# Kernel tuning notes

Hardware: AMD Instinct MI355X
Metric: run time of the kernel (lower is better)

## Reference

```python
import jax, jax.numpy as jnp
import numpy as np

EPS = 1e-5

def _bn(x, g, b):
    # BatchNorm1d in training mode: biased batch variance, eps=1e-5
    mu = jnp.mean(x, axis=0)
    var = jnp.var(x, axis=0)
    return g * (x - mu) * jax.lax.rsqrt(var + EPS) + b

def _prelu(x, a):
    return jnp.where(x >= 0, x, a * x)

def setup_inputs() -> dict:
    key = jax.random.key(0)
    ks = jax.random.split(key, 32)
    B, MF, E = 4096, 128, 64
    f32 = jnp.float32

    def lin_w(k, o, i):
        bound = 1.0 / np.sqrt(i)
        return jax.random.uniform(k, (o, i), f32, -bound, bound)

    def lin_b(k, o, i):
        bound = 1.0 / np.sqrt(i)
        return jax.random.uniform(k, (o,), f32, -bound, bound)

    def exp_w(k, e, o, i):
        bound = 1.0 / np.sqrt(i)
        return jax.random.uniform(k, (e, o, i), f32, -bound, bound)

    def exp_b(k, e, o, i):
        bound = 1.0 / np.sqrt(i)
        return jax.random.uniform(k, (e, o), f32, -bound, bound)

    quarter = jnp.full((1,), 0.25, f32)  # PReLU default init
    return {
        'm0': jax.random.normal(ks[0], (B, MF), f32),
        'x0': jax.random.normal(ks[1], (B, 64), f32),
        'mW1': lin_w(ks[2], 256, 128), 'mb1': lin_b(ks[3], 256, 128),
        'mg1': jnp.ones((256,), f32), 'mbe1': jnp.zeros((256,), f32), 'ma1': quarter,
        'mW2': lin_w(ks[4], 128, 256), 'mb2': lin_b(ks[5], 128, 256),
        'mg2': jnp.ones((128,), f32), 'mbe2': jnp.zeros((128,), f32), 'ma2': quarter,
        'mW3': lin_w(ks[6], 64, 128), 'mb3': lin_b(ks[7], 64, 128),
        'mg3': jnp.ones((64,), f32), 'mbe3': jnp.zeros((64,), f32), 'ma3': quarter,
        'Wenc0': exp_w(ks[8], E, 256, 64), 'benc0': exp_b(ks[9], E, 256, 64),
        'Wenc1': exp_w(ks[10], E, 256, 256), 'benc1': exp_b(ks[11], E, 256, 256),
        'Wdec0': exp_w(ks[12], E, 256, 256), 'bdec0': exp_b(ks[13], E, 256, 256),
        'Wdec1': exp_w(ks[14], E, 64, 256), 'bdec1': exp_b(ks[15], E, 64, 256),
        'bng': jnp.ones((256,), f32), 'bnb': jnp.zeros((256,), f32), 'a': quarter,
    }

def reference(m0, x0, mW1, mb1, mg1, mbe1, ma1, mW2, mb2, mg2, mbe2, ma2,
              mW3, mb3, mg3, mbe3, ma3, Wenc0, benc0, Wenc1, benc1,
              Wdec0, bdec0, Wdec1, bdec1, bng, bnb, a):
    # m_encoder (MNet): Linear+BN+PReLU x3 -> per-sample expert weights [B, 64]
    h = _prelu(_bn(m0 @ mW1.T + mb1, mg1, mbe1), ma1)
    h = _prelu(_bn(h @ mW2.T + mb2, mg2, mbe2), ma2)
    w = _prelu(_bn(h @ mW3.T + mb3, mg3, mbe3), ma3)  # [B, E]

    w_sum = jnp.sum(w)           # scalar sum over all B*E, as in torch code
    wn = w / w_sum               # [B, E]

    def experts(z, W, b):
        # all-experts dense combine: sum_e wn[b,e] * (z @ W_e^T + b_e)
        h = jnp.einsum('bi,eoi->beo', z, W) + b  # [B, E, O]
        return jnp.einsum('beo,be->bo', h, wn)

    # encoder: depth=2, BN+PReLU after each layer (shared bn(256) and PReLU)
    z = _prelu(_bn(experts(x0, Wenc0, benc0), bng, bnb), a)
    z = _prelu(_bn(experts(z, Wenc1, benc1), bng, bnb), a)
    # decoder: BN+PReLU on all but last layer
    y = _prelu(_bn(experts(z, Wdec0, bdec0), bng, bnb), a)
    y = experts(y, Wdec1, bdec1)  # [B, 64]
    return y
```

## Files before the change

### kernel.cpp

```cpp
#include <hip/hip_runtime.h>
#include <stdint.h>

#define BATCH 4096
#define NEXP 64

typedef __bf16 bf16x8 __attribute__((ext_vector_type(8)));
typedef _Float16 f16x8 __attribute__((ext_vector_type(8)));
typedef float f32x4 __attribute__((ext_vector_type(4)));
typedef float f32x8 __attribute__((ext_vector_type(8)));
typedef unsigned int u32x4 __attribute__((ext_vector_type(4)));
typedef unsigned short u16x4 __attribute__((ext_vector_type(4)));
typedef unsigned short u16x8 __attribute__((ext_vector_type(8)));

__device__ __forceinline__ unsigned short f2bf(float f) {
  unsigned u = __builtin_bit_cast(unsigned, f);
  u += 0x7fffu + ((u >> 16) & 1u);
  return (unsigned short)(u >> 16);
}
__device__ __forceinline__ float bf2f(unsigned short h) {
  unsigned u = ((unsigned)h) << 16;
  return __builtin_bit_cast(float, u);
}
__device__ __forceinline__ unsigned short f2h(float f) {
  return __builtin_bit_cast(unsigned short, (_Float16)f);
}

__device__ __forceinline__ void async_copy16(const void* g, void* l) {
  __builtin_amdgcn_global_load_lds(
      (const __attribute__((address_space(1))) void*)(uintptr_t)g,
      (__attribute__((address_space(3))) void*)(uintptr_t)l, 16, 0, 0);
}

enum { AM_PLAIN = 0, AM_BN = 1 };

template <int BM_, int BN_, int WR, int WC, int AMODE>
__global__ __launch_bounds__(256, 4) void gemm_k(
    const float* __restrict__ Af32, const float* __restrict__ scv,
    const float* __restrict__ shv, const float* __restrict__ alphaPtr,
    const unsigned short* __restrict__ PB, int K, int nsubsTot,
    float* __restrict__ Cp, const float* __restrict__ biasv, int N,
    int ktilesTot) {
  constexpr int MS = BM_ / 16;
  constexpr int NS = BN_ / 16;
  constexpr int WTM = BM_ / WR, WTN = BN_ / WC;
  constexpr int TM = WTM / 16, TN = WTN / 16;
  constexpr int PCH = MS / 2;

  __shared__ __align__(16) unsigned short As[2 * MS * 512];
  __shared__ __align__(16) unsigned short Bs[2 * NS * 512];

  const int tid = threadIdx.x;
  const int lane = tid & 63;
  const int wid = tid >> 6;
  const int wrow = wid / WC, wcol = wid % WC;

  const int m0 = blockIdx.x * BM_;
  const int ntile = blockIdx.y;
  const int n0 = ntile * BN_;

  float alpha = 0.f;
  if constexpr (AMODE == AM_BN) alpha = alphaPtr[0];

  f32x4 acc[TM][TN] = {};

  for (int kt = 0; kt < ktilesTot; ++kt) {
    const int k0 = kt * 64;

    for (int f = wid; f < 2 * NS; f += 4) {
      const int fkt = f / NS, fns = f % NS;
      const long fragIdx = (long)(k0 / 32 + fkt) * nsubsTot + (ntile * NS + fns);
      async_copy16(PB + fragIdx * 512 + lane * 8, &Bs[f * 512 + lane * 8]);
    }

#pragma unroll
    for (int p = 0; p < PCH; ++p) {
      const int id = p * 256 + tid;
      const int fA = id >> 6;
      const int q = id & 63;
      const int ksh = fA / MS, msub = fA % MS;
      const int kq = q >> 4, mrow = q & 15;
      const int m = msub * 16 + mrow;
      const int kg = k0 + ksh * 32 + kq * 8;
      const long mg = m0 + m;
      f32x8 vf;
      if constexpr (AMODE == AM_PLAIN) {
        const f32x4* src = (const f32x4*)(Af32 + mg * K + kg);
        f32x4 a0 = src[0], a1 = src[1];
#pragma unroll
        for (int j = 0; j < 4; ++j) { vf[j] = a0[j]; vf[4 + j] = a1[j]; }
      } else {
        const f32x4* src = (const f32x4*)(Af32 + mg * K + kg);
        f32x4 a0 = src[0], a1 = src[1];
        f32x4 s0 = *(const f32x4*)(scv + kg), s1 = *(const f32x4*)(scv + kg + 4);
        f32x4 h0 = *(const f32x4*)(shv + kg), h1 = *(const f32x4*)(shv + kg + 4);
#pragma unroll
        for (int j = 0; j < 4; ++j) {
          float v = fmaf(a0[j], s0[j], h0[j]);
          vf[j] = v >= 0.f ? v : alpha * v;
          float v2 = fmaf(a1[j], s1[j], h1[j]);
          vf[4 + j] = v2 >= 0.f ? v2 : alpha * v2;
        }
      }
      bf16x8 ob = __builtin_convertvector(vf, bf16x8);
      *(u16x8*)&As[id * 8] = __builtin_bit_cast(u16x8, ob);
    }
    __syncthreads();

#pragma unroll
    for (int ks = 0; ks < 2; ++ks) {
      bf16x8 af[TM], bfr[TN];
#pragma unroll
      for (int i = 0; i < TM; ++i) {
        const int msub = wrow * TM + i;
        af[i] = __builtin_bit_cast(
            bf16x8, *(const u32x4*)&As[(ks * MS + msub) * 512 + lane * 8]);
      }
#pragma unroll
      for (int j = 0; j < TN; ++j) {
        const int nsub = wcol * TN + j;
        bfr[j] = __builtin_bit_cast(
            bf16x8, *(const u32x4*)&Bs[(ks * NS + nsub) * 512 + lane * 8]);
      }
#pragma unroll
      for (int i = 0; i < TM; ++i)
#pragma unroll
        for (int j = 0; j < TN; ++j)
          acc[i][j] = __builtin_amdgcn_mfma_f32_16x16x32_bf16(af[i], bfr[j],
                                                              acc[i][j], 0, 0, 0);
    }
    __syncthreads();
  }

  const int q = lane >> 4, nn = lane & 15;
#pragma unroll
  for (int i = 0; i < TM; ++i) {
    const int rowb = m0 + wrow * WTM + i * 16 + q * 4;
#pragma unroll
    for (int j = 0; j < TN; ++j) {
      const int col = n0 + wcol * WTN + j * 16 + nn;
      const float bv = biasv ? biasv[col] : 0.f;
#pragma unroll
      for (int r = 0; r < 4; ++r)
        Cp[(long)(rowb + r) * N + col] = acc[i][j][r] + bv;
    }
  }
}

template <int BN_, int KE_, int EPB, int NTILE, int KHALVES>
__global__ __launch_bounds__(256, 2) void egemm_k(
    const unsigned short* __restrict__ zpk, const float* __restrict__ wnT,
    const float* __restrict__ bias, const unsigned short* __restrict__ PB,
    float* __restrict__ Cbase, long partStride, int N, int nsubsTot) {
  constexpr int KT2F = KE_ / 32;
  constexpr int KT2 = KT2F / KHALVES;
  constexpr int LK = (KT2 == 8) ? 3 : (KT2 == 4) ? 2 : 1;
  constexpr int NS = BN_ / 16;
  constexpr int TN = NS / 4;
  constexpr int TM = 4;
  constexpr int S = NEXP / EPB;
  constexpr int NC = NTILE * S * KHALVES;
  constexpr int T = EPB * KT2;
  constexpr int U = ((KT2 & 3) == 0) ? 1 : (4 / KT2);

  __shared__ __align__(16) unsigned short As[KT2 * 4 * 512];

  const int tid = threadIdx.x, lane = tid & 63, wid = tid >> 6;
  const int bx = blockIdx.x;
  const int combo = bx % NC;
  const int mb = bx / NC;
  const int ntile = combo % NTILE;
  const int rest = combo / NTILE;
  const int slice = rest % S;
  const int khalf = rest / S;
  const int e0 = slice * EPB;
  const int n0 = ntile * BN_;
  float* __restrict__ Cp = Cbase + (long)(khalf * S + slice) * partStride;
  const int nn = lane & 15, q = lane >> 4;
  const bool addBias = (KHALVES == 1) || (khalf == 0);

  {
    const unsigned short* zb =
        zpk + (long)mb * (KT2F * 4 * 512) + (long)khalf * (KT2 * 4 * 512);
    for (int f = wid; f < KT2 * 4; f += 4)
      async_copy16(zb + f * 512 + lane * 8, &As[f * 512 + lane * 8]);
  }

  const long kstr = (long)nsubsTot * 512;
  const unsigned short* Bq = PB + ((long)e0 * KT2F + khalf * KT2) * kstr +
                             ((long)ntile * NS + wid * TN) * 512 + lane * 8;
  auto baddr = [&](int u) {
    const int ei = u >> LK, kt = u & (KT2 - 1);
    return Bq + ((long)ei * KT2F + kt) * kstr;
  };

  u32x4 ring[4][TN];
#pragma unroll
  for (int t = 0; t < 4; ++t) {
    const unsigned short* a = baddr(t < T ? t : T - 1);
#pragma unroll
    for (int j = 0; j < TN; ++j) ring[t][j] = *(const u32x4*)(a + j * 512);
  }

  __syncthreads();

  f32x4 mainAcc[TM][TN] = {};

  for (int eb = 0; eb < EPB; eb += U) {
#pragma unroll
    for (int uu = 0; uu < U; ++uu) {
      const int ei = eb + uu;
      const int e = e0 + ei;
      f32x4 tmp[TM][TN];
#pragma unroll
      for (int j = 0; j < TN; ++j) {
        const float bv =
            addBias ? bias[(long)e * N + n0 + wid * (TN * 16) + j * 16 + nn]
                    : 0.f;
        f32x4 t4 = {bv, bv, bv, bv};
#pragma unroll
        for (int i = 0; i < TM; ++i) tmp[i][j] = t4;
      }
#pragma unroll
      for (int kt = 0; kt < KT2; ++kt) {
        const int slot = (uu * KT2 + kt) & 3;
#pragma unroll
        for (int i = 0; i < TM; ++i) {
          f16x8 af = __builtin_bit_cast(
              f16x8, *(const u32x4*)&As[(kt * 4 + i) * 512 + lane * 8]);
#pragma unroll
          for (int j = 0; j < TN; ++j)
            tmp[i][j] = __builtin_amdgcn_mfma_f32_16x16x32_f16(
                af, __builtin_bit_cast(f16x8, ring[slot][j]), tmp[i][j], 0, 0,
                0);
        }
        {
          const int u = ei * KT2 + kt;
          const int un = (u + 4 < T) ? (u + 4) : (T - 1);
          const unsigned short* a = baddr(un);
#pragma unroll
          for (int j = 0; j < TN; ++j)
            ring[slot][j] = *(const u32x4*)(a + j * 512);
        }
      }
#pragma unroll
      for (int i = 0; i < TM; ++i) {
        const int rowb = mb * 64 + i * 16 + q * 4;
        f32x4 wn4 = *(const f32x4*)(wnT + (long)e * BATCH + rowb);
#pragma unroll
        for (int j = 0; j < TN; ++j) mainAcc[i][j] += wn4 * tmp[i][j];
      }
    }
  }

#pragma unroll
  for (int i = 0; i < TM; ++i) {
    const int rowb = mb * 64 + i * 16 + q * 4;
#pragma unroll
    for (int j = 0; j < TN; ++j) {
      const int col = n0 + wid * (TN * 16) + j * 16 + nn;
#pragma unroll
      for (int r = 0; r < 4; ++r)
        Cp[(long)(rowb + r) * N + col] = mainAcc[i][j][r];
    }
  }
}

template <int EPB>
__global__ __launch_bounds__(256, 1) void egemm2_k(
    const unsigned short* __restrict__ zpk, const float* __restrict__ wnT,
    const float* __restrict__ bias, const unsigned short* __restrict__ PB,
    unsigned short* __restrict__ Pb, long partStrideH) {
  constexpr int TM = 8, TN = 4;
  constexpr int S = NEXP / EPB;
  constexpr int T = EPB * 8;

  __shared__ __align__(16) unsigned short As[8 * 8 * 512];

  const int tid = threadIdx.x, lane = tid & 63, wid = tid >> 6;
  const int bx = blockIdx.x;
  const int slice = bx % S;
  const int mb = bx / S;
  const int e0 = slice * EPB;
  const int nn = lane & 15, q = lane >> 4;

  for (int f = wid; f < 64; f += 4) {
    const int kt = f >> 3, msub = f & 7;
    const unsigned short* src =
        zpk + ((long)(2 * mb + (msub >> 2)) * 32 + kt * 4 + (msub & 3)) * 512;
    async_copy16(src + lane * 8, &As[f * 512 + lane * 8]);
  }

  const long kstr = 16L * 512;
  const unsigned short* Bq =
      PB + (long)e0 * 8 * kstr + ((long)wid * TN) * 512 + lane * 8;

  u32x4 ring[4][TN];
#pragma unroll
  for (int t = 0; t < 4; ++t)
#pragma unroll
    for (int j = 0; j < TN; ++j)
      ring[t][j] = *(const u32x4*)(Bq + (long)t * kstr + j * 512);

  __syncthreads();

  f32x4 acc[TM][TN] = {};

  for (int ei = 0; ei < EPB; ++ei) {
    const int e = e0 + ei;
    f16x8 wnh[TM];
#pragma unroll
    for (int i = 0; i < TM; ++i) {
      const float w =
          wnT[(long)e * BATCH + mb * 128 + i * 16 + (lane & 15)] * 4096.f;
      const _Float16 h = (_Float16)w;
      f16x8 v = {h, h, h, h, h, h, h, h};
      wnh[i] = v;
    }
#pragma unroll
    for (int kt = 0; kt < 8; ++kt) {
      const int slot = kt & 3;
#pragma unroll
      for (int i = 0; i < TM; ++i) {
        f16x8 af = __builtin_bit_cast(
            f16x8, *(const u32x4*)&As[(kt * 8 + i) * 512 + lane * 8]);
        f16x8 afs = af * wnh[i];
#pragma unroll
        for (int j = 0; j < TN; ++j)
          acc[i][j] = __builtin_amdgcn_mfma_f32_16x16x32_f16(
              afs, __builtin_bit_cast(f16x8, ring[slot][j]), acc[i][j], 0, 0,
              0);
      }
      {
        const int u = ei * 8 + kt;
        const int un = (u + 4 < T) ? (u + 4) : (T - 1);
#pragma unroll
        for (int j = 0; j < TN; ++j)
          ring[slot][j] = *(const u32x4*)(Bq + (long)un * kstr + j * 512);
      }
    }
  }

#pragma unroll
  for (int i = 0; i < TM; ++i)
#pragma unroll
    for (int j = 0; j < TN; ++j) acc[i][j] *= (1.f / 4096.f);
  for (int ei = 0; ei < EPB; ++ei) {
    const int e = e0 + ei;
    float bs[TN];
#pragma unroll
    for (int j = 0; j < TN; ++j)
      bs[j] = bias[(long)e * 256 + wid * 64 + j * 16 + nn];
#pragma unroll
    for (int i = 0; i < TM; ++i) {
      f32x4 wn4 =
          *(const f32x4*)(wnT + (long)e * BATCH + mb * 128 + i * 16 + q * 4);
#pragma unroll
      for (int j = 0; j < TN; ++j) acc[i][j] += wn4 * bs[j];
    }
  }
  unsigned short* Cp = Pb + (long)slice * partStrideH;
#pragma unroll
  for (int i = 0; i < TM; ++i) {
    const int rowb = mb * 128 + i * 16 + q * 4;
#pragma unroll
    for (int j = 0; j < TN; ++j) {
      const int col = wid * 64 + j * 16 + nn;
#pragma unroll
      for (int r = 0; r < 4; ++r)
        Cp[(long)(rowb + r) * 256 + col] = f2bf(acc[i][j][r]);
    }
  }
}

template <int NPARTS>
__global__ void hstats_k(float* __restrict__ P, long partStride,
                         f32x4* __restrict__ BS1, f32x4* __restrict__ BS2) {
  const int c0 = (threadIdx.x & 63) * 4;
  const int rg = threadIdx.x >> 6;
  const int rb = blockIdx.x * 8;
  f32x4 s = {0.f, 0.f, 0.f, 0.f}, s2 = {0.f, 0.f, 0.f, 0.f};
#pragma unroll
  for (int it = 0; it < 2; ++it) {
    const long r = rb + it * 4 + rg;
    f32x4 v[NPARTS];
#pragma unroll
    for (int p = 0; p < NPARTS; ++p)
      v[p] = *(const f32x4*)(P + p * partStride + r * 256 + c0);
    f32x4 x = v[0];
#pragma unroll
    for (int p = 1; p < NPARTS; ++p) x += v[p];
    *(f32x4*)(P + r * 256 + c0) = x;
    s += x;
    s2 += x * x;
  }
  __shared__ f32x4 sb[256], qb[256];
  sb[threadIdx.x] = s;
  qb[threadIdx.x] = s2;
  __syncthreads();
  if (threadIdx.x < 64) {
    f32x4 ts = sb[threadIdx.x] + sb[64 + threadIdx.x] + sb[128 + threadIdx.x] +
               sb[192 + threadIdx.x];
    f32x4 tq = qb[threadIdx.x] + qb[64 + threadIdx.x] + qb[128 + threadIdx.x] +
               qb[192 + threadIdx.x];
    BS1[threadIdx.x * 512 + blockIdx.x] = ts;
    BS2[threadIdx.x * 512 + blockIdx.x] = tq;
  }
}

__global__ void hstats16_k(const unsigned short* __restrict__ P,
                           long partStrideH, float* __restrict__ H,
                           f32x4* __restrict__ BS1, f32x4* __restrict__ BS2) {
  const int c0 = (threadIdx.x & 63) * 4;
  const int rg = threadIdx.x >> 6;
  const int rb = blockIdx.x * 8;
  f32x4 s = {0.f, 0.f, 0.f, 0.f}, s2 = {0.f, 0.f, 0.f, 0.f};
#pragma unroll
  for (int it = 0; it < 2; ++it) {
    const long r = rb + it * 4 + rg;
    u16x4 v[8];
#pragma unroll
    for (int p = 0; p < 8; ++p)
      v[p] = *(const u16x4*)(P + p * partStrideH + r * 256 + c0);
    f32x4 x = {0.f, 0.f, 0.f, 0.f};
#pragma unroll
    for (int p = 0; p < 8; ++p)
#pragma unroll
      for (int j = 0; j < 4; ++j) x[j] += bf2f(v[p][j]);
    *(f32x4*)(H + r * 256 + c0) = x;
    s += x;
    s2 += x * x;
  }
  __shared__ f32x4 sb[256], qb[256];
  sb[threadIdx.x] = s;
  qb[threadIdx.x] = s2;
  __syncthreads();
  if (threadIdx.x < 64) {
    f32x4 ts = sb[threadIdx.x] + sb[64 + threadIdx.x] + sb[128 + threadIdx.x] +
               sb[192 + threadIdx.x];
    f32x4 tq = qb[threadIdx.x] + qb[64 + threadIdx.x] + qb[128 + threadIdx.x] +
               qb[192 + threadIdx.x];
    BS1[threadIdx.x * 512 + blockIdx.x] = ts;
    BS2[threadIdx.x * 512 + blockIdx.x] = tq;
  }
}

__global__ void sfin_k(const f32x4* __restrict__ BS1,
                       const f32x4* __restrict__ BS2,
                       const float* __restrict__ g, const float* __restrict__ b,
                       float* __restrict__ scv, float* __restrict__ shv) {
  const int cg = blockIdx.x;
  f32x4 s1 = BS1[cg * 512 + threadIdx.x] + BS1[cg * 512 + 256 + threadIdx.x];
  f32x4 s2 = BS2[cg * 512 + threadIdx.x] + BS2[cg * 512 + 256 + threadIdx.x];
  __shared__ f32x4 sb[256], qb[256];
  sb[threadIdx.x] = s1;
  qb[threadIdx.x] = s2;
  __syncthreads();
  for (int st = 128; st > 0; st >>= 1) {
    if (threadIdx.x < st) {
      sb[threadIdx.x] += sb[threadIdx.x + st];
      qb[threadIdx.x] += qb[threadIdx.x + st];
    }
    __syncthreads();
  }
  if (threadIdx.x < 4) {
    const int c = cg * 4 + threadIdx.x;
    float mu = sb[0][threadIdx.x] * (1.f / BATCH);
    float var = qb[0][threadIdx.x] * (1.f / BATCH) - mu * mu;
    float isig = 1.f / sqrtf(var + 1e-5f);
    float sc_ = g[c] * isig;
    scv[c] = sc_;
    shv[c] = b[c] - mu * sc_;
  }
}

__global__ void stats_k(const float* __restrict__ H, int C,
                        const float* __restrict__ g, const float* __restrict__ b,
                        float* __restrict__ scv, float* __restrict__ shv) {
  const int c0 = blockIdx.x * 4;
  f32x4 s = {0.f, 0.f, 0.f, 0.f}, s2 = {0.f, 0.f, 0.f, 0.f};
  for (int r = threadIdx.x; r < BATCH; r += 256) {
    f32x4 x = *(const f32x4*)(H + (long)r * C + c0);
    s += x;
    s2 += x * x;
  }
  __shared__ f32x4 sb[256], qb[256];
  sb[threadIdx.x] = s;
  qb[threadIdx.x] = s2;
  __syncthreads();
  for (int st = 128; st > 0; st >>= 1) {
    if (threadIdx.x < st) {
      sb[threadIdx.x] += sb[threadIdx.x + st];
      qb[threadIdx.x] += qb[threadIdx.x + st];
    }
    __syncthreads();
  }
  if (threadIdx.x < 4) {
    const int c = c0 + threadIdx.x;
    float mu = sb[0][threadIdx.x] * (1.f / BATCH);
    float var = qb[0][threadIdx.x] * (1.f / BATCH) - mu * mu;
    float isig = 1.f / sqrtf(var + 1e-5f);
    float sc_ = g[c] * isig;
    scv[c] = sc_;
    shv[c] = b[c] - mu * sc_;
  }
}

__global__ void zbuild_pk(const float* __restrict__ H,
                          const float* __restrict__ scv,
                          const float* __restrict__ shv,
                          const float* __restrict__ alphaPtr,
                          unsigned short* __restrict__ zpk) {
  const int c = blockIdx.x * 256 + threadIdx.x;
  const float alpha = alphaPtr[0];
  const int mb = c >> 11, r = c & 2047;
  const int kt = r >> 8, q2 = r & 255;
  const int msub = q2 >> 6, ln = q2 & 63;
  const int row = mb * 64 + msub * 16 + (ln & 15);
  const int col = kt * 32 + (ln >> 4) * 8;
  const float* src = H + (long)row * 256 + col;
  f32x4 a0 = *(const f32x4*)src, a1 = *(const f32x4*)(src + 4);
  f32x4 s0 = *(const f32x4*)(scv + col), s1 = *(const f32x4*)(scv + col + 4);
  f32x4 h0 = *(const f32x4*)(shv + col), h1 = *(const f32x4*)(shv + col + 4);
  u16x8 o;
#pragma unroll
  for (int j = 0; j < 4; ++j) {
    float v = fmaf(a0[j], s0[j], h0[j]);
    v = v >= 0.f ? v : alpha * v;
    o[j] = f2h(v);
    float v2 = fmaf(a1[j], s1[j], h1[j]);
    v2 = v2 >= 0.f ? v2 : alpha * v2;
    o[4 + j] = f2h(v2);
  }
  *(u16x8*)(zpk + (long)c * 8) = o;
}

__global__ void wbuild_k(const float* __restrict__ G, const float* __restrict__ scv,
                         const float* __restrict__ shv,
                         const float* __restrict__ alphaPtr,
                         float* __restrict__ w, float* __restrict__ wps) {
  const int idx = blockIdx.x * 256 + threadIdx.x;
  const float alpha = alphaPtr[0];
  const int c0 = (idx * 4) & 63;
  f32x4 x = *(const f32x4*)(G + (long)idx * 4);
  f32x4 sv = *(const f32x4*)(scv + c0);
  f32x4 hv = *(const f32x4*)(shv + c0);
  f32x4 o;
  float part = 0.f;
#pragma unroll
  for (int j = 0; j < 4; ++j) {
    float v = fmaf(x[j], sv[j], hv[j]);
    v = v >= 0.f ? v : alpha * v;
    o[j] = v;
    part += v;
  }
  *(f32x4*)(w + (long)idx * 4) = o;
  __shared__ float sb[256];
  sb[threadIdx.x] = part;
  __syncthreads();
  for (int st = 128; st > 0; st >>= 1) {
    if (threadIdx.x < st) sb[threadIdx.x] += sb[threadIdx.x + st];
    __syncthreads();
  }
  if (threadIdx.x == 0) wps[blockIdx.x] = sb[0];
}

__global__ void wnTcast_k(const float* __restrict__ w,
                          const float* __restrict__ wps,
                          float* __restrict__ wnT, const float* __restrict__ x0,
                          unsigned short* __restrict__ x0pk) {
  const int bx = blockIdx.x;
  if (bx < 1024) {
    __shared__ float sb[256];
    sb[threadIdx.x] = wps[threadIdx.x];
    __syncthreads();
    for (int st = 128; st > 0; st >>= 1) {
      if (threadIdx.x < st) sb[threadIdx.x] += sb[threadIdx.x + st];
      __syncthreads();
    }
    const float inv = 1.0f / sb[0];
    const int idx = bx * 256 + threadIdx.x;
    const int e = idx >> 12, b2 = idx & 4095;
    wnT[idx] = w[(long)b2 * NEXP + e] * inv;
  } else {
    const int c = (bx - 1024) * 256 + threadIdx.x;
    const int mb = c >> 9, r = c & 511;
    const int kt = r >> 8, q2 = r & 255;
    const int msub = q2 >> 6, ln = q2 & 63;
    const int row = mb * 64 + msub * 16 + (ln & 15);
    const int col = kt * 32 + (ln >> 4) * 8;
    const float* src = x0 + (long)row * 64 + col;
    f32x4 a0 = *(const f32x4*)src, a1 = *(const f32x4*)(src + 4);
    u16x8 o;
#pragma unroll
    for (int j = 0; j < 4; ++j) {
      o[j] = f2h(a0[j]);
      o[4 + j] = f2h(a1[j]);
    }
    *(u16x8*)(x0pk + (long)c * 8) = o;
  }
}

__global__ void mnetprep_k(const float* __restrict__ w0,
                           const float* __restrict__ w1,
                           const float* __restrict__ w2,
                           unsigned short* __restrict__ PB) {
  const int t = blockIdx.x * 256 + threadIdx.x;
  const float* W;
  int nsubs, shI;
  long loc;
  if (t < 4096) { W = w0; nsubs = 16; shI = 7; loc = t; }
  else if (t < 8192) { W = w1; nsubs = 8; shI = 8; loc = t - 4096; }
  else if (t < 9216) { W = w2; nsubs = 4; shI = 7; loc = t - 8192; }
  else return;
  const int lane = (int)(loc & 63);
  const long frag = loc >> 6;
  const int nsub = (int)(frag % nsubs);
  const long ktile = frag / nsubs;
  const int n = nsub * 16 + (lane & 15);
  const int k = (int)(ktile * 32 + (lane >> 4) * 8);
  const int e = k >> shI;
  const int i0 = k & ((1 << shI) - 1);
  const int O = nsubs * 16;
  const float* src = W + ((long)e * O + n) * (1 << shI) + i0;
  f32x4 a0 = *(const f32x4*)src, a1 = *(const f32x4*)(src + 4);
  u16x8 o;
#pragma unroll
  for (int j = 0; j < 4; ++j) {
    o[j] = f2bf(a0[j]);
    o[4 + j] = f2bf(a1[j]);
  }
  *(u16x8*)(PB + (long)t * 8) = o;
}

__global__ void eprep_k(const float* __restrict__ W,
                        unsigned short* __restrict__ PB, int nsubs, int shI,
                        long totalChunks) {
  const long t = (long)blockIdx.x * 256 + threadIdx.x;
  if (t >= totalChunks) return;
  const int lane = (int)(t & 63);
  const long frag = t >> 6;
  const int nsub = (int)(frag % nsubs);
  const long ktile = frag / nsubs;
  const int n = nsub * 16 + (lane & 15);
  const int k = (int)(ktile * 32 + (lane >> 4) * 8);
  const int e = k >> shI;
  const int i0 = k & ((1 << shI) - 1);
  const int O = nsubs * 16;
  const float* src = W + ((long)e * O + n) * (1 << shI) + i0;
  f32x4 a0 = *(const f32x4*)src, a1 = *(const f32x4*)(src + 4);
  u16x8 o;
#pragma unroll
  for (int j = 0; j < 4; ++j) {
    o[j] = f2h(a0[j]);
    o[4 + j] = f2h(a1[j]);
  }
  *(u16x8*)(PB + (long)t * 8) = o;
}

template <int NP>
__global__ void reduceN_k(const float* __restrict__ P, long partStride,
                          float* __restrict__ out, int total4) {
  const int idx = blockIdx.x * 256 + threadIdx.x;
  if (idx >= total4) return;
  f32x4 v[NP];
#pragma unroll
  for (int p = 0; p < NP; ++p)
    v[p] = *(const f32x4*)(P + p * partStride + (long)idx * 4);
  f32x4 s = v[0];
#pragma unroll
  for (int p = 1; p < NP; ++p) s += v[p];
  *(f32x4*)(out + (long)idx * 4) = s;
}

extern "C" void kernel_launch(void* const* d_in, const int* in_sizes, int n_in,
                              void* d_out, int out_size, void* d_ws, size_t ws_size,
                              hipStream_t stream) {
  const float* m0 = (const float*)d_in[0];
  const float* x0 = (const float*)d_in[1];
  const float* mW1 = (const float*)d_in[2];
  const float* mb1 = (const float*)d_in[3];
  const float* mg1 = (const float*)d_in[4];
  const float* mbe1 = (const float*)d_in[5];
  const float* ma1 = (const float*)d_in[6];
  const float* mW2 = (const float*)d_in[7];
  const float* mb2 = (const float*)d_in[8];
  const float* mg2 = (const float*)d_in[9];
  const float* mbe2 = (const float*)d_in[10];
  const float* ma2 = (const float*)d_in[11];
  const float* mW3 = (const float*)d_in[12];
  const float* mb3 = (const float*)d_in[13];
  const float* mg3 = (const float*)d_in[14];
  const float* mbe3 = (const float*)d_in[15];
  const float* ma3 = (const float*)d_in[16];
  const float* Wenc0 = (const float*)d_in[17];
  const float* benc0 = (const float*)d_in[18];
  const float* Wenc1 = (const float*)d_in[19];
  const float* benc1 = (const float*)d_in[20];
  const float* Wdec0 = (const float*)d_in[21];
  const float* bdec0 = (const float*)d_in[22];
  const float* Wdec1 = (const float*)d_in[23];
  const float* bdec1 = (const float*)d_in[24];
  const float* bng = (const float*)d_in[25];
  const float* bnb = (const float*)d_in[26];
  const float* aexp = (const float*)d_in[27];

  const long PSP32 = (long)BATCH * 256 + 64;
  const long PSPH = (long)BATCH * 256 + 128;
  const long PSD = (long)BATCH * 64 + 64;

  char* base = (char*)d_ws;
  size_t off = 0;
  auto alloc = [&](size_t bytes) {
    void* p = base + off;
    off = (off + bytes + 255) & ~(size_t)255;
    return p;
  };
  unsigned short* PBm = (unsigned short*)alloc(9216L * 16);
  unsigned short* PBe = (unsigned short*)alloc(524288L * 16);
  size_t pbBytes = 16UL * PSD * 4;
  if (8UL * PSPH * 2 > pbBytes) pbBytes = 8UL * PSPH * 2;
  if (4UL * PSP32 * 4 > pbBytes) pbBytes = 4UL * PSP32 * 4;
  void* PbBase = alloc(pbBytes);
  float* Pb32 = (float*)PbBase;
  unsigned short* Pb16 = (unsigned short*)PbBase;
  float* P0 = Pb32;
  float* P1 = Pb32 + (long)BATCH * 256;
  float* Hbuf = (float*)alloc((size_t)BATCH * 256 * 4);
  unsigned short* zApk = (unsigned short*)alloc(BATCH * 256 * 2);
  unsigned short* zBpk = (unsigned short*)alloc(BATCH * 256 * 2);
  unsigned short* x0pk = (unsigned short*)alloc(BATCH * 64 * 2);
  float* wbuf = (float*)alloc(BATCH * 64 * 4);
  float* wnT = (float*)alloc((size_t)NEXP * BATCH * 4);
  f32x4* BS1 = (f32x4*)alloc(64 * 512 * 16);
  f32x4* BS2 = (f32x4*)alloc(64 * 512 * 16);
  float* scv = (float*)alloc(256 * 4);
  float* shv = (float*)alloc(256 * 4);
  float* wps = (float*)alloc(256 * 4);

  const dim3 blk(256);

  mnetprep_k<<<36, blk, 0, stream>>>(mW1, mW2, mW3, PBm);

  gemm_k<64, 128, 2, 2, AM_PLAIN><<<dim3(64, 2, 1), blk, 0, stream>>>(
      m0, nullptr, nullptr, nullptr, PBm, 128, 16, P0, mb1, 256, 2);
  stats_k<<<64, blk, 0, stream>>>(P0, 256, mg1, mbe1, scv, shv);
  gemm_k<64, 128, 2, 2, AM_BN><<<dim3(64, 1, 1), blk, 0, stream>>>(
      P0, scv, shv, ma1, PBm + 4096L * 8, 256, 8, P1, mb2, 128, 4);
  stats_k<<<32, blk, 0, stream>>>(P1, 128, mg2, mbe2, scv, shv);
  gemm_k<64, 64, 2, 2, AM_BN><<<dim3(64, 1, 1), blk, 0, stream>>>(
      P1, scv, shv, ma2, PBm + 8192L * 8, 128, 4, P0, mb3, 64, 2);
  stats_k<<<16, blk, 0, stream>>>(P0, 64, mg3, mbe3, scv, shv);
  wbuild_k<<<256, blk, 0, stream>>>(P0, scv, shv, ma3, wbuf, wps);
  wnTcast_k<<<1152, blk, 0, stream>>>(wbuf, wps, wnT, x0, x0pk);

  eprep_k<<<512, blk, 0, stream>>>(Wenc0, PBe, 16, 6, 131072);
  egemm_k<128, 64, 16, 2, 1><<<dim3(512), blk, 0, stream>>>(
      x0pk, wnT, benc0, PBe, Pb32, PSP32, 256, 16);
  hstats_k<4><<<512, blk, 0, stream>>>(Pb32, PSP32, BS1, BS2);
  sfin_k<<<64, blk, 0, stream>>>(BS1, BS2, bng, bnb, scv, shv);
  zbuild_pk<<<512, blk, 0, stream>>>(Pb32, scv, shv, aexp, zApk);

  eprep_k<<<2048, blk, 0, stream>>>(Wenc1, PBe, 16, 8, 524288);
  egemm2_k<8><<<dim3(256), blk, 0, stream>>>(zApk, wnT, benc1, PBe, Pb16, PSPH);
  hstats16_k<<<512, blk, 0, stream>>>(Pb16, PSPH, Hbuf, BS1, BS2);
  sfin_k<<<64, blk, 0, stream>>>(BS1, BS2, bng, bnb, scv, shv);
  zbuild_pk<<<512, blk, 0, stream>>>(Hbuf, scv, shv, aexp, zBpk);

  eprep_k<<<2048, blk, 0, stream>>>(Wdec0, PBe, 16, 8, 524288);
  egemm2_k<8><<<dim3(256), blk, 0, stream>>>(zBpk, wnT, bdec0, PBe, Pb16, PSPH);
  hstats16_k<<<512, blk, 0, stream>>>(Pb16, PSPH, Hbuf, BS1, BS2);
  sfin_k<<<64, blk, 0, stream>>>(BS1, BS2, bng, bnb, scv, shv);
  zbuild_pk<<<512, blk, 0, stream>>>(Hbuf, scv, shv, aexp, zApk);

  eprep_k<<<512, blk, 0, stream>>>(Wdec1, PBe, 4, 8, 131072);
  egemm_k<64, 256, 8, 1, 2><<<dim3(1024), blk, 0, stream>>>(
      zApk, wnT, bdec1, PBe, Pb32, PSD, 64, 4);
  reduceN_k<16><<<256, blk, 0, stream>>>(Pb32, PSD, (float*)d_out, 65536);

  (void)in_sizes; (void)n_in; (void)out_size; (void)ws_size;
}
```

Baseline: 358.9 us.

## Split egemm2 K dimension across blocks and fuse partial reduction into zbuild

Result: slower. 471.2 us (+31.3%).

```diff
diff --git a/kernel.cpp b/kernel.cpp
--- a/kernel.cpp
+++ b/kernel.cpp
@@ -265,41 +265,49 @@
   }
 }
 
-template <int EPB>
-__global__ __launch_bounds__(256, 1) void egemm2_k(
+__global__ __launch_bounds__(256, 2) void egemm2_k(
     const unsigned short* __restrict__ zpk, const float* __restrict__ wnT,
     const float* __restrict__ bias, const unsigned short* __restrict__ PB,
     unsigned short* __restrict__ Pb, long partStrideH) {
   constexpr int TM = 8, TN = 4;
-  constexpr int S = NEXP / EPB;
-  constexpr int T = EPB * 8;
-
-  __shared__ __align__(16) unsigned short As[8 * 8 * 512];
+  constexpr int EPB = 8, S = 8;
+  constexpr int NC = S * 2;
+  constexpr int T = EPB * 4;
+
+  __shared__ __align__(16) unsigned short As[4 * 8 * 512];
 
   const int tid = threadIdx.x, lane = tid & 63, wid = tid >> 6;
   const int bx = blockIdx.x;
-  const int slice = bx % S;
-  const int mb = bx / S;
+  const int combo = bx % NC;
+  const int mb = bx / NC;
+  const int slice = combo % S;
+  const int khalf = combo / S;
   const int e0 = slice * EPB;
   const int nn = lane & 15, q = lane >> 4;
 
-  for (int f = wid; f < 64; f += 4) {
+  for (int f = wid; f < 32; f += 4) {
     const int kt = f >> 3, msub = f & 7;
+    const int ktg = khalf * 4 + kt;
     const unsigned short* src =
-        zpk + ((long)(2 * mb + (msub >> 2)) * 32 + kt * 4 + (msub & 3)) * 512;
+        zpk + ((long)(2 * mb + (msub >> 2)) * 32 + ktg * 4 + (msub & 3)) * 512;
     async_copy16(src + lane * 8, &As[f * 512 + lane * 8]);
   }
 
   const long kstr = 16L * 512;
-  const unsigned short* Bq =
-      PB + (long)e0 * 8 * kstr + ((long)wid * TN) * 512 + lane * 8;
+  const unsigned short* Bq = PB + ((long)e0 * 8 + khalf * 4) * kstr +
+                             ((long)wid * TN) * 512 + lane * 8;
+  auto baddr = [&](int u) {
+    const int ei = u >> 2, kt = u & 3;
+    return Bq + ((long)ei * 8 + kt) * kstr;
+  };
 
   u32x4 ring[4][TN];
 #pragma unroll
-  for (int t = 0; t < 4; ++t)
-#pragma unroll
-    for (int j = 0; j < TN; ++j)
-      ring[t][j] = *(const u32x4*)(Bq + (long)t * kstr + j * 512);
+  for (int t = 0; t < 4; ++t) {
+    const unsigned short* a = baddr(t);
+#pragma unroll
+    for (int j = 0; j < TN; ++j) ring[t][j] = *(const u32x4*)(a + j * 512);
+  }
 
   __syncthreads();
 
@@ -310,15 +318,14 @@
     f16x8 wnh[TM];
 #pragma unroll
     for (int i = 0; i < TM; ++i) {
-      const float w =
-          wnT[(long)e * BATCH + mb * 128 + i * 16 + (lane & 15)] * 4096.f;
+      const float w = wnT[(long)e * BATCH + mb * 128 + i * 16 + nn] * 4096.f;
       const _Float16 h = (_Float16)w;
       f16x8 v = {h, h, h, h, h, h, h, h};
       wnh[i] = v;
     }
 #pragma unroll
-    for (int kt = 0; kt < 8; ++kt) {
-      const int slot = kt & 3;
+    for (int kt = 0; kt < 4; ++kt) {
+      const int slot = kt;
 #pragma unroll
       for (int i = 0; i < TM; ++i) {
         f16x8 af = __builtin_bit_cast(
@@ -331,11 +338,12 @@
               0);
       }
       {
-        const int u = ei * 8 + kt;
+        const int u = ei * 4 + kt;
         const int un = (u + 4 < T) ? (u + 4) : (T - 1);
+        const unsigned short* a = baddr(un);
 #pragma unroll
         for (int j = 0; j < TN; ++j)
-          ring[slot][j] = *(const u32x4*)(Bq + (long)un * kstr + j * 512);
+          ring[slot][j] = *(const u32x4*)(a + j * 512);
       }
     }
   }
@@ -344,21 +352,23 @@
   for (int i = 0; i < TM; ++i)
 #pragma unroll
     for (int j = 0; j < TN; ++j) acc[i][j] *= (1.f / 4096.f);
-  for (int ei = 0; ei < EPB; ++ei) {
-    const int e = e0 + ei;
-    float bs[TN];
-#pragma unroll
-    for (int j = 0; j < TN; ++j)
-      bs[j] = bias[(long)e * 256 + wid * 64 + j * 16 + nn];
-#pragma unroll
-    for (int i = 0; i < TM; ++i) {
-      f32x4 wn4 =
-          *(const f32x4*)(wnT + (long)e * BATCH + mb * 128 + i * 16 + q * 4);
-#pragma unroll
-      for (int j = 0; j < TN; ++j) acc[i][j] += wn4 * bs[j];
-    }
-  }
-  unsigned short* Cp = Pb + (long)slice * partStrideH;
+  if (khalf == 0) {
+    for (int ei = 0; ei < EPB; ++ei) {
+      const int e = e0 + ei;
+      float bs[TN];
+#pragma unroll
+      for (int j = 0; j < TN; ++j)
+        bs[j] = bias[(long)e * 256 + wid * 64 + j * 16 + nn];
+#pragma unroll
+      for (int i = 0; i < TM; ++i) {
+        f32x4 wn4 =
+            *(const f32x4*)(wnT + (long)e * BATCH + mb * 128 + i * 16 + q * 4);
+#pragma unroll
+        for (int j = 0; j < TN; ++j) acc[i][j] += wn4 * bs[j];
+      }
+    }
+  }
+  unsigned short* Cp = Pb + (long)(khalf * S + slice) * partStrideH;
 #pragma unroll
   for (int i = 0; i < TM; ++i) {
     const int rowb = mb * 128 + i * 16 + q * 4;
@@ -408,8 +418,8 @@
 }
 
 __global__ void hstats16_k(const unsigned short* __restrict__ P,
-                           long partStrideH, float* __restrict__ H,
-                           f32x4* __restrict__ BS1, f32x4* __restrict__ BS2) {
+                           long partStrideH, f32x4* __restrict__ BS1,
+                           f32x4* __restrict__ BS2) {
   const int c0 = (threadIdx.x & 63) * 4;
   const int rg = threadIdx.x >> 6;
   const int rb = blockIdx.x * 8;
@@ -417,16 +427,15 @@
 #pragma unroll
   for (int it = 0; it < 2; ++it) {
     const long r = rb + it * 4 + rg;
-    u16x4 v[8];
-#pragma unroll
-    for (int p = 0; p < 8; ++p)
+    u16x4 v[16];
+#pragma unroll
+    for (int p = 0; p < 16; ++p)
       v[p] = *(const u16x4*)(P + p * partStrideH + r * 256 + c0);
     f32x4 x = {0.f, 0.f, 0.f, 0.f};
 #pragma unroll
-    for (int p = 0; p < 8; ++p)
+    for (int p = 0; p < 16; ++p)
 #pragma unroll
       for (int j = 0; j < 4; ++j) x[j] += bf2f(v[p][j]);
-    *(f32x4*)(H + r * 256 + c0) = x;
     s += x;
     s2 += x * x;
   }
@@ -528,6 +537,41 @@
     v = v >= 0.f ? v : alpha * v;
     o[j] = f2h(v);
     float v2 = fmaf(a1[j], s1[j], h1[j]);
+    v2 = v2 >= 0.f ? v2 : alpha * v2;
+    o[4 + j] = f2h(v2);
+  }
+  *(u16x8*)(zpk + (long)c * 8) = o;
+}
+
+__global__ void zbuild16_pk(const unsigned short* __restrict__ P,
+                            long partStrideH, const float* __restrict__ scv,
+                            const float* __restrict__ shv,
+                            const float* __restrict__ alphaPtr,
+                            unsigned short* __restrict__ zpk) {
+  const int c = blockIdx.x * 256 + threadIdx.x;
+  const float alpha = alphaPtr[0];
+  const int mb = c >> 11, r = c & 2047;
+  const int kt = r >> 8, q2 = r & 255;
+  const int msub = q2 >> 6, ln = q2 & 63;
+  const int row = mb * 64 + msub * 16 + (ln & 15);
+  const int col = kt * 32 + (ln >> 4) * 8;
+  const long base = (long)row * 256 + col;
+  float s[8] = {0.f, 0.f, 0.f, 0.f, 0.f, 0.f, 0.f, 0.f};
+#pragma unroll
+  for (int p = 0; p < 16; ++p) {
+    u16x8 v = *(const u16x8*)(P + p * partStrideH + base);
+#pragma unroll
+    for (int j = 0; j < 8; ++j) s[j] += bf2f(v[j]);
+  }
+  f32x4 s0 = *(const f32x4*)(scv + col), s1 = *(const f32x4*)(scv + col + 4);
+  f32x4 h0 = *(const f32x4*)(shv + col), h1 = *(const f32x4*)(shv + col + 4);
+  u16x8 o;
+#pragma unroll
+  for (int j = 0; j < 4; ++j) {
+    float v = fmaf(s[j], s0[j], h0[j]);
+    v = v >= 0.f ? v : alpha * v;
+    o[j] = f2h(v);
+    float v2 = fmaf(s[4 + j], s1[j], h1[j]);
     v2 = v2 >= 0.f ? v2 : alpha * v2;
     o[4 + j] = f2h(v2);
   }
@@ -717,15 +761,14 @@
   };
   unsigned short* PBm = (unsigned short*)alloc(9216L * 16);
   unsigned short* PBe = (unsigned short*)alloc(524288L * 16);
-  size_t pbBytes = 16UL * PSD * 4;
-  if (8UL * PSPH * 2 > pbBytes) pbBytes = 8UL * PSPH * 2;
+  size_t pbBytes = 16UL * PSPH * 2;
   if (4UL * PSP32 * 4 > pbBytes) pbBytes = 4UL * PSP32 * 4;
+  if (16UL * PSD * 4 > pbBytes) pbBytes = 16UL * PSD * 4;
   void* PbBase = alloc(pbBytes);
   float* Pb32 = (float*)PbBase;
   unsigned short* Pb16 = (unsigned short*)PbBase;
   float* P0 = Pb32;
   float* P1 = Pb32 + (long)BATCH * 256;
-  float* Hbuf = (float*)alloc((size_t)BATCH * 256 * 4);
   unsigned short* zApk = (unsigned short*)alloc(BATCH * 256 * 2);
   unsigned short* zBpk = (unsigned short*)alloc(BATCH * 256 * 2);
   unsigned short* x0pk = (unsigned short*)alloc(BATCH * 64 * 2);
@@ -761,16 +804,16 @@
   zbuild_pk<<<512, blk, 0, stream>>>(Pb32, scv, shv, aexp, zApk);
 
   eprep_k<<<2048, blk, 0, stream>>>(Wenc1, PBe, 16, 8, 524288);
-  egemm2_k<8><<<dim3(256), blk, 0, stream>>>(zApk, wnT, benc1, PBe, Pb16, PSPH);
-  hstats16_k<<<512, blk, 0, stream>>>(Pb16, PSPH, Hbuf, BS1, BS2);
+  egemm2_k<<<dim3(512), blk, 0, stream>>>(zApk, wnT, benc1, PBe, Pb16, PSPH);
+  hstats16_k<<<512, blk, 0, stream>>>(Pb16, PSPH, BS1, BS2);
   sfin_k<<<64, blk, 0, stream>>>(BS1, BS2, bng, bnb, scv, shv);
-  zbuild_pk<<<512, blk, 0, stream>>>(Hbuf, scv, shv, aexp, zBpk);
+  zbuild16_pk<<<512, blk, 0, stream>>>(Pb16, PSPH, scv, shv, aexp, zBpk);
 
   eprep_k<<<2048, blk, 0, stream>>>(Wdec0, PBe, 16, 8, 524288);
-  egemm2_k<8><<<dim3(256), blk, 0, stream>>>(zBpk, wnT, bdec0, PBe, Pb16, PSPH);
-  hstats16_k<<<512, blk, 0, stream>>>(Pb16, PSPH, Hbuf, BS1, BS2);
+  egemm2_k<<<dim3(512), blk, 0, stream>>>(zBpk, wnT, bdec0, PBe, Pb16, PSPH);
+  hstats16_k<<<512, blk, 0, stream>>>(Pb16, PSPH, BS1, BS2);
   sfin_k<<<64, blk, 0, stream>>>(BS1, BS2, bng, bnb, scv, shv);
-  zbuild_pk<<<512, blk, 0, stream>>>(Hbuf, scv, shv, aexp, zApk);
+  zbuild16_pk<<<512, blk, 0, stream>>>(Pb16, PSPH, scv, shv, aexp, zApk);
 
   eprep_k<<<512, blk, 0, stream>>>(Wdec1, PBe, 4, 8, 131072);
   egemm_k<64, 256, 8, 1, 2><<<dim3(1024), blk, 0, stream>>>(
```
